# Performance work log

Measured on AMD Instinct MI355X. Metric: run time of the kernel, lower is better.

Reference implementation:

```python
import jax, jax.numpy as jnp
import numpy as np

B, S = 64, 1024
D_INPUT, D_POLAR, N_LAYERS, KAN, N_CLASSES = 256, 256, 8, 32, 1000
PI = float(np.pi)
EPS = 1e-8


def _gelu(v):
    return jax.nn.gelu(v, approximate=False)  # torch nn.GELU default = exact erf


def setup_inputs() -> dict:
    key = jax.random.key(0)
    ks = jax.random.split(key, 16)

    def rn(k, shape, fan_in):
        return jax.random.normal(k, shape, jnp.float32) / np.sqrt(fan_in)

    return {
        "x": jax.random.normal(ks[0], (B, S, D_INPUT), jnp.float32),
        "embed_w": rn(ks[1], (D_INPUT, 2 * D_POLAR), D_INPUT),
        "embed_b": jnp.zeros((2 * D_POLAR,), jnp.float32),
        "mag_w1": rn(ks[2], (N_LAYERS, 1, KAN), 1),
        "mag_b1": jnp.zeros((N_LAYERS, KAN), jnp.float32),
        "mag_w2": rn(ks[3], (N_LAYERS, KAN, 1), KAN),
        "mag_b2": jnp.zeros((N_LAYERS, 1), jnp.float32),
        "ph_w1": rn(ks[4], (N_LAYERS, 2, KAN), 2),
        "ph_b1": jnp.zeros((N_LAYERS, KAN), jnp.float32),
        "ph_w2": rn(ks[5], (N_LAYERS, KAN, 2), KAN),
        "ph_b2": jnp.zeros((N_LAYERS, 2), jnp.float32),
        "cls_w1": rn(ks[6], (D_POLAR, KAN), D_POLAR),
        "cls_b1": jnp.zeros((KAN,), jnp.float32),
        "cls_w2": rn(ks[7], (KAN, N_CLASSES), KAN),
        "cls_b2": jnp.zeros((N_CLASSES,), jnp.float32),
    }


def _forward(x, embed_w, embed_b, mag_w1, mag_b1, mag_w2, mag_b2,
             ph_w1, ph_b1, ph_w2, ph_b2, cls_w1, cls_b1, cls_w2, cls_b2):
    h = x @ embed_w + embed_b                      # [B,S,2D]
    r = jnp.abs(h[..., :D_POLAR]) + 0.1            # [B,S,D]
    theta = h[..., D_POLAR:] * PI                  # [B,S,D]
    for i in range(N_LAYERS):
        xc = r * jnp.cos(theta)
        yc = r * jnp.sin(theta)
        xm = xc.mean(axis=1, keepdims=True)        # [B,1,D]
        ym = yc.mean(axis=1, keepdims=True)
        r_agg = jnp.sqrt(xm * xm + ym * ym + EPS)
        th_agg = jnp.arctan2(ym, xm)
        # magnitude MLP (1 -> 32 -> 1) in log space, per channel
        log_r = jnp.log(r_agg + EPS)[..., None]    # [B,1,D,1]
        lr = _gelu(log_r @ mag_w1[i] + mag_b1[i]) @ mag_w2[i] + mag_b2[i]
        r_trans = jnp.exp(lr[..., 0])              # [B,1,D]
        # phase MLP (2 -> 32 -> 2) on (sin, cos)
        pin = jnp.stack([jnp.sin(th_agg), jnp.cos(th_agg)], axis=-1)  # [B,1,D,2]
        pout = _gelu(pin @ ph_w1[i] + ph_b1[i]) @ ph_w2[i] + ph_b2[i]
        norm = jnp.sqrt(pout[..., 0] ** 2 + pout[..., 1] ** 2 + EPS)
        th_trans = jnp.arctan2(pout[..., 0] / norm, pout[..., 1] / norm)
        x_out = xc + r_trans * jnp.cos(th_trans)
        y_out = yc + r_trans * jnp.sin(th_trans)
        r = jnp.sqrt(x_out * x_out + y_out * y_out + EPS)
        theta = jnp.arctan2(y_out, x_out)
    pooled = r.mean(axis=1)                        # [B,D]
    return _gelu(pooled @ cls_w1 + cls_b1) @ cls_w2 + cls_b2  # [B,n_classes]


def reference(x, embed_w, embed_b, mag_w1, mag_b1, mag_w2, mag_b2,
              ph_w1, ph_b1, ph_w2, ph_b2, cls_w1, cls_b1, cls_w2, cls_b2):
    return _forward(x, embed_w, embed_b, mag_w1, mag_b1, mag_w2, mag_b2,
                    ph_w1, ph_b1, ph_w2, ph_b2, cls_w1, cls_b1, cls_w2, cls_b2)
```

## Files before the change

kernel.cpp:

```cpp
#include <hip/hip_runtime.h>
#include <hip/hip_bf16.h>
#include <hip/hip_fp16.h>

#define EPS 1e-8f
#define PI_F 3.14159265358979323846f

typedef _Float16 half8 __attribute__((ext_vector_type(8)));
typedef _Float16 half4 __attribute__((ext_vector_type(4)));
typedef float f32x4 __attribute__((ext_vector_type(4)));
typedef float f32x2 __attribute__((ext_vector_type(2)));

__device__ __forceinline__ float gelu_exact(float v) {
    return 0.5f * v * (1.0f + erff(v * 0.70710678118654752f));
}

__global__ void convertW(const float* __restrict__ W,
                         _Float16* __restrict__ Wth, _Float16* __restrict__ Wtl,
                         float* __restrict__ zero_base) {
    int idx = blockIdx.x * 256 + threadIdx.x;
    if (idx < 49152) zero_base[idx] = 0.f;
    int col = idx & 511, k = idx >> 9;
    int d  = col & 255;
    int g  = d >> 6;
    int dl = d & 63;
    int r  = (dl >> 5) * 64 + ((col >> 8) << 5) + (dl & 31);
    int kt = k >> 5, ko = k & 31;
    float f = W[k * 512 + col];
    _Float16 h = (_Float16)f;
    int o = ((g * 8 + kt) * 128 + r) * 32 + ko;
    Wth[o] = h;
    Wtl[o] = (_Float16)(f - (float)h);
}

__global__ __launch_bounds__(256, 4) void gemm_embed(
    const float* __restrict__ x,
    const _Float16* __restrict__ Wth, const _Float16* __restrict__ Wtl,
    const float* __restrict__ bias,
    unsigned short* __restrict__ XY8,
    float* __restrict__ XMsum, float* __restrict__ YMsum)
{
    __shared__ __attribute__((aligned(16))) _Float16 Ah[4096], Al[4096];
    const int tid  = threadIdx.x;
    const int wave = tid >> 6;
    const int lane = tid & 63;
    const int wm   = wave >> 1;
    const int wn   = wave & 1;
    const int id   = blockIdx.x;
    const int xcd  = id & 7;
    const int s    = id >> 3;
    const int g    = s & 3;
    const int mt   = (s >> 2) * 8 + xcd;
    const int m0   = mt * 128;
    const int q    = lane >> 4, ln = lane & 15;

    f32x4 acc[4][4];
#pragma unroll
    for (int mi = 0; mi < 4; ++mi)
#pragma unroll
        for (int nt = 0; nt < 4; ++nt)
            acc[mi][nt] = (f32x4){0.f, 0.f, 0.f, 0.f};

    for (int kt = 0; kt < 8; ++kt) {
        half8 bh[4], bl[4];
        {
            const int tbase = (g * 8 + kt) * 4096;
#pragma unroll
            for (int nt = 0; nt < 4; ++nt) {
                int off = tbase + (wn * 64 + nt * 16 + ln) * 32 + q * 8;
                bh[nt] = *(const half8*)(Wth + off);
                bl[nt] = *(const half8*)(Wtl + off);
            }
        }
        __syncthreads();
#pragma unroll
        for (int L = 0; L < 2; ++L) {
            int idx2 = L * 256 + tid;
            int r = idx2 >> 2, cq = idx2 & 3;
            const float* src = x + (size_t)(m0 + r) * 256 + kt * 32 + cq * 8;
            const float4 f0 = *(const float4*)(src);
            const float4 f1 = *(const float4*)(src + 4);
            half8 hh, ll;
            hh[0] = (_Float16)f0.x; ll[0] = (_Float16)(f0.x - (float)hh[0]);
            hh[1] = (_Float16)f0.y; ll[1] = (_Float16)(f0.y - (float)hh[1]);
            hh[2] = (_Float16)f0.z; ll[2] = (_Float16)(f0.z - (float)hh[2]);
            hh[3] = (_Float16)f0.w; ll[3] = (_Float16)(f0.w - (float)hh[3]);
            hh[4] = (_Float16)f1.x; ll[4] = (_Float16)(f1.x - (float)hh[4]);
            hh[5] = (_Float16)f1.y; ll[5] = (_Float16)(f1.y - (float)hh[5]);
            hh[6] = (_Float16)f1.z; ll[6] = (_Float16)(f1.z - (float)hh[6]);
            hh[7] = (_Float16)f1.w; ll[7] = (_Float16)(f1.w - (float)hh[7]);
            int pos = cq ^ ((r >> 1) & 3);
            *(half8*)&Ah[r * 32 + pos * 8] = hh;
            *(half8*)&Al[r * 32 + pos * 8] = ll;
        }
        __syncthreads();

        half8 am[4];
#pragma unroll
        for (int mi = 0; mi < 4; ++mi) {
            int row = wm * 64 + mi * 16 + ln;
            am[mi] = *(const half8*)&Ah[row * 32 + (q ^ ((row >> 1) & 3)) * 8];
        }
#pragma unroll
        for (int mi = 0; mi < 4; ++mi)
#pragma unroll
            for (int nt = 0; nt < 4; ++nt)
                acc[mi][nt] = __builtin_amdgcn_mfma_f32_16x16x32_f16(am[mi], bh[nt], acc[mi][nt], 0, 0, 0);
#pragma unroll
        for (int mi = 0; mi < 4; ++mi)
#pragma unroll
            for (int nt = 0; nt < 4; ++nt)
                acc[mi][nt] = __builtin_amdgcn_mfma_f32_16x16x32_f16(am[mi], bl[nt], acc[mi][nt], 0, 0, 0);
#pragma unroll
        for (int mi = 0; mi < 4; ++mi) {
            int row = wm * 64 + mi * 16 + ln;
            half8 alv = *(const half8*)&Al[row * 32 + (q ^ ((row >> 1) & 3)) * 8];
#pragma unroll
            for (int nt = 0; nt < 4; ++nt)
                acc[mi][nt] = __builtin_amdgcn_mfma_f32_16x16x32_f16(alv, bh[nt], acc[mi][nt], 0, 0, 0);
        }
    }

    const int d0 = g * 64 + wn * 32 + ln;
    const int d1 = d0 + 16;
    const int b  = m0 >> 10;
    const float b1_0 = bias[d0],       b1_1 = bias[d1];
    const float b2_0 = bias[256 + d0], b2_1 = bias[256 + d1];
    float sx0 = 0.f, sy0 = 0.f, sx1 = 0.f, sy1 = 0.f;
#pragma unroll
    for (int mi = 0; mi < 4; ++mi) {
#pragma unroll
        for (int i = 0; i < 4; ++i) {
            const int row = m0 + wm * 64 + mi * 16 + q * 4 + i;
            {
                const float h1 = acc[mi][0][i] + b1_0;
                const float h2 = acc[mi][2][i] + b2_0;
                const float rr = fabsf(h1) + 0.1f;
                float sv, cv;
                __sincosf(PI_F * h2, &sv, &cv);
                const float xc = rr * cv, yc = rr * sv;
                int pk = __builtin_amdgcn_cvt_pk_fp8_f32(xc, yc, 0, false);
                XY8[(size_t)row * 256 + d0] = (unsigned short)pk;
                sx0 += xc; sy0 += yc;
            }
            {
                const float h1 = acc[mi][1][i] + b1_1;
                const float h2 = acc[mi][3][i] + b2_1;
                const float rr = fabsf(h1) + 0.1f;
                float sv, cv;
                __sincosf(PI_F * h2, &sv, &cv);
                const float xc = rr * cv, yc = rr * sv;
                int pk = __builtin_amdgcn_cvt_pk_fp8_f32(xc, yc, 0, false);
                XY8[(size_t)row * 256 + d1] = (unsigned short)pk;
                sx1 += xc; sy1 += yc;
            }
        }
    }
    sx0 += __shfl_down(sx0, 32); sx0 += __shfl_down(sx0, 16);
    sy0 += __shfl_down(sy0, 32); sy0 += __shfl_down(sy0, 16);
    sx1 += __shfl_down(sx1, 32); sx1 += __shfl_down(sx1, 16);
    sy1 += __shfl_down(sy1, 32); sy1 += __shfl_down(sy1, 16);
    if (lane < 16) {
        atomicAdd(&XMsum[b * 256 + d0], sx0);
        atomicAdd(&YMsum[b * 256 + d0], sy0);
        atomicAdd(&XMsum[b * 256 + d1], sx1);
        atomicAdd(&YMsum[b * 256 + d1], sy1);
    }
}

__global__ __launch_bounds__(256) void layers_kernel(
    const float* __restrict__ XMsum, const float* __restrict__ YMsum,
    const float* __restrict__ mw1, const float* __restrict__ mb1,
    const float* __restrict__ mw2, const float* __restrict__ mb2,
    const float* __restrict__ pw1, const float* __restrict__ pb1,
    const float* __restrict__ pw2, const float* __restrict__ pb2,
    float* __restrict__ DX, float* __restrict__ DY)
{
    __shared__ float s_mw1[256], s_mb1[256], s_mw2[256], s_mb2[8];
    __shared__ float s_pw1[512], s_pb1[256], s_pw2[512], s_pb2[16];
    const int tid = threadIdx.x;
    s_mw1[tid] = mw1[tid]; s_mb1[tid] = mb1[tid];
    s_mw2[tid] = mw2[tid]; s_pb1[tid] = pb1[tid];
    s_pw1[tid] = pw1[tid]; s_pw1[256 + tid] = pw1[256 + tid];
    s_pw2[tid] = pw2[tid]; s_pw2[256 + tid] = pw2[256 + tid];
    if (tid < 8)  s_mb2[tid] = mb2[tid];
    if (tid < 16) s_pb2[tid] = pb2[tid];
    __syncthreads();

    const int gid = blockIdx.x * 256 + tid;
    const int idx = gid >> 3;
    const int sub = gid & 7;
    float xm = XMsum[idx] * (1.0f / 1024.0f);
    float ym = YMsum[idx] * (1.0f / 1024.0f);
    float dxa = 0.f, dya = 0.f;
#pragma unroll 1
    for (int i = 0; i < 8; ++i) {
        float r2    = xm * xm + ym * ym;
        float r_agg = sqrtf(r2 + EPS);
        float hyp   = sqrtf(r2);
        float inv   = hyp > 0.f ? 1.0f / hyp : 0.f;
        float st    = ym * inv;
        float ct    = hyp > 0.f ? xm * inv : 1.0f;
        float log_r = logf(r_agg + EPS);
        float lr = 0.f, p0 = 0.f, p1 = 0.f;
#pragma unroll
        for (int k4 = 0; k4 < 4; ++k4) {
            int k = sub * 4 + k4;
            float hm = gelu_exact(log_r * s_mw1[i * 32 + k] + s_mb1[i * 32 + k]);
            lr += hm * s_mw2[i * 32 + k];
            float hp = gelu_exact(st * s_pw1[i * 64 + k] + ct * s_pw1[i * 64 + 32 + k] + s_pb1[i * 32 + k]);
            p0 += hp * s_pw2[i * 64 + 2 * k + 0];
            p1 += hp * s_pw2[i * 64 + 2 * k + 1];
        }
        lr += __shfl_xor(lr, 1); lr += __shfl_xor(lr, 2); lr += __shfl_xor(lr, 4);
        p0 += __shfl_xor(p0, 1); p0 += __shfl_xor(p0, 2); p0 += __shfl_xor(p0, 4);
        p1 += __shfl_xor(p1, 1); p1 += __shfl_xor(p1, 2); p1 += __shfl_xor(p1, 4);
        lr += s_mb2[i];
        p0 += s_pb2[i * 2 + 0];
        p1 += s_pb2[i * 2 + 1];
        float r_trans = expf(lr);
        float hp2  = sqrtf(p0 * p0 + p1 * p1);
        float invp = hp2 > 0.f ? 1.0f / hp2 : 0.f;
        float ctt  = hp2 > 0.f ? p1 * invp : 1.0f;
        float stt  = p0 * invp;
        float dx = r_trans * ctt;
        float dy = r_trans * stt;
        dxa += dx; dya += dy; xm += dx; ym += dy;
    }
    if (sub == 0) { DX[idx] = dxa; DY[idx] = dya; }
}

__global__ __launch_bounds__(256) void pool_kernel(
    const unsigned short* __restrict__ XY8,
    const float* __restrict__ DX, const float* __restrict__ DY,
    float* __restrict__ pooled)
{
    __shared__ float red[256][9];
    const int b = blockIdx.x, sc = blockIdx.y, tid = threadIdx.x;
    const int dg = tid & 31;
    const int sh = tid >> 5;
    const int d0 = dg * 8;
    float dxv[8], dyv[8], s[8];
#pragma unroll
    for (int j = 0; j < 8; ++j) {
        dxv[j] = DX[b * 256 + d0 + j];
        dyv[j] = DY[b * 256 + d0 + j];
        s[j] = 0.f;
    }
    const int r0 = sc * 128 + sh * 16;
    const size_t base = ((size_t)b * 1024 + r0) * 256 + d0;
#pragma unroll 4
    for (int i = 0; i < 16; ++i) {
        const int4 v = *(const int4*)(XY8 + base + (size_t)i * 256);
        const int wv[4] = {v.x, v.y, v.z, v.w};
#pragma unroll
        for (int w = 0; w < 4; ++w) {
            f32x2 pa = __builtin_amdgcn_cvt_pk_f32_fp8(wv[w], false);
            f32x2 pb = __builtin_amdgcn_cvt_pk_f32_fp8(wv[w], true);
            float xa = pa[0] + dxv[2 * w],     ya = pa[1] + dyv[2 * w];
            float xb = pb[0] + dxv[2 * w + 1], yb = pb[1] + dyv[2 * w + 1];
            s[2 * w]     += sqrtf(xa * xa + ya * ya + EPS);
            s[2 * w + 1] += sqrtf(xb * xb + yb * yb + EPS);
        }
    }
#pragma unroll
    for (int j = 0; j < 8; ++j) red[tid][j] = s[j];
    __syncthreads();
    if (tid < 32) {
#pragma unroll
        for (int j = 0; j < 8; ++j) {
            float t = 0.f;
#pragma unroll
            for (int c = 0; c < 8; ++c) t += red[c * 32 + tid][j];
            atomicAdd(&pooled[b * 256 + tid * 8 + j], t);
        }
    }
}

__global__ __launch_bounds__(256) void cls_kernel(
    const float* __restrict__ pooled,
    const float* __restrict__ w1, const float* __restrict__ b1,
    const float* __restrict__ w2, const float* __restrict__ b2,
    float* __restrict__ out)
{
    __shared__ float pl[256];
    __shared__ float part[8][32];
    __shared__ float hd[32];
    const int b = blockIdx.x, yc = blockIdx.y, tid = threadIdx.x;
    pl[tid] = pooled[b * 256 + tid] * (1.0f / 1024.0f);
    __syncthreads();
    const int hu = tid & 31, kc = tid >> 5;
    float a = 0.f;
    for (int k = kc * 32; k < kc * 32 + 32; ++k) a += pl[k] * w1[k * 32 + hu];
    part[kc][hu] = a;
    __syncthreads();
    if (tid < 32) {
        float s = b1[tid];
#pragma unroll
        for (int c = 0; c < 8; ++c) s += part[c][tid];
        hd[tid] = gelu_exact(s);
    }
    __syncthreads();
    const int n0 = yc * 250;
    const int nend = (n0 + 250 < 1000) ? n0 + 250 : 1000;
    for (int n = n0 + tid; n < nend; n += 256) {
        float s = b2[n];
#pragma unroll
        for (int k = 0; k < 32; ++k) s += hd[k] * w2[k * 1000 + n];
        out[b * 1000 + n] = s;
    }
}

extern "C" void kernel_launch(void* const* d_in, const int* in_sizes, int n_in,
                              void* d_out, int out_size, void* d_ws, size_t ws_size,
                              hipStream_t stream)
{
    const float* x       = (const float*)d_in[0];
    const float* embed_w = (const float*)d_in[1];
    const float* embed_b = (const float*)d_in[2];
    const float* mag_w1  = (const float*)d_in[3];
    const float* mag_b1  = (const float*)d_in[4];
    const float* mag_w2  = (const float*)d_in[5];
    const float* mag_b2  = (const float*)d_in[6];
    const float* ph_w1   = (const float*)d_in[7];
    const float* ph_b1   = (const float*)d_in[8];
    const float* ph_w2   = (const float*)d_in[9];
    const float* ph_b2   = (const float*)d_in[10];
    const float* cls_w1  = (const float*)d_in[11];
    const float* cls_b1  = (const float*)d_in[12];
    const float* cls_w2  = (const float*)d_in[13];
    const float* cls_b2  = (const float*)d_in[14];
    float* out = (float*)d_out;

    char* ws = (char*)d_ws;
    unsigned short* XY8 = (unsigned short*)(ws + 0);
    _Float16* Wth = (_Float16*)(ws + 33554432);
    _Float16* Wtl = (_Float16*)(ws + 33816576);
    float* XMsum  = (float*)(ws + 34078720);
    float* YMsum  = (float*)(ws + 34144256);
    float* pooled = (float*)(ws + 34209792);
    float* DX     = (float*)(ws + 34275328);
    float* DY     = (float*)(ws + 34340864);

    convertW<<<512, 256, 0, stream>>>(embed_w, Wth, Wtl, XMsum);
    gemm_embed<<<2048, 256, 0, stream>>>(x, Wth, Wtl, embed_b, XY8, XMsum, YMsum);
    layers_kernel<<<512, 256, 0, stream>>>(XMsum, YMsum, mag_w1, mag_b1, mag_w2, mag_b2,
                                           ph_w1, ph_b1, ph_w2, ph_b2, DX, DY);
    pool_kernel<<<dim3(64, 8), 256, 0, stream>>>(XY8, DX, DY, pooled);
    cls_kernel<<<dim3(64, 4), 256, 0, stream>>>(pooled, cls_w1, cls_b1, cls_w2, cls_b2, out);
}
```

Baseline: 204.2 us.

## Double-buffer embed GEMM LDS with register prefetch and pack paired fp8 stores

The embed GEMM now ping-pongs between two LDS buffers and prefetches the next k-tile of x into registers while the current tile is converted and consumed. This drops one barrier per k-step and hides global load latency. The weight column layout is permuted so each lane owns two adjacent channels, which lets the epilogue pack both channels' fp8 pairs into a single 32-bit store instead of two 16-bit stores. LDS use doubles and the launch bound drops from 4 to 3 blocks per CU, so occupancy may fall.

```diff
diff --git a/kernel.cpp b/kernel.cpp
--- a/kernel.cpp
+++ b/kernel.cpp
@@ -20,11 +20,12 @@
     int idx = blockIdx.x * 256 + threadIdx.x;
     if (idx < 49152) zero_base[idx] = 0.f;
     int col = idx & 511, k = idx >> 9;
-    int d  = col & 255;
-    int g  = d >> 6;
-    int dl = d & 63;
-    int r  = (dl >> 5) * 64 + ((col >> 8) << 5) + (dl & 31);
-    int kt = k >> 5, ko = k & 31;
+    int d   = col & 255;
+    int g   = d >> 6;
+    int dl  = d & 63;
+    int h12 = col >> 8;
+    int r   = (dl >> 5) * 64 + ((dl & 1) + 2 * h12) * 16 + ((dl & 31) >> 1);
+    int kt  = k >> 5, ko = k & 31;
     float f = W[k * 512 + col];
     _Float16 h = (_Float16)f;
     int o = ((g * 8 + kt) * 128 + r) * 32 + ko;
@@ -32,14 +33,14 @@
     Wtl[o] = (_Float16)(f - (float)h);
 }
 
-__global__ __launch_bounds__(256, 4) void gemm_embed(
+__global__ __launch_bounds__(256, 3) void gemm_embed(
     const float* __restrict__ x,
     const _Float16* __restrict__ Wth, const _Float16* __restrict__ Wtl,
     const float* __restrict__ bias,
     unsigned short* __restrict__ XY8,
     float* __restrict__ XMsum, float* __restrict__ YMsum)
 {
-    __shared__ __attribute__((aligned(16))) _Float16 Ah[4096], Al[4096];
+    __shared__ __attribute__((aligned(16))) _Float16 Ah[2][4096], Al[2][4096];
     const int tid  = threadIdx.x;
     const int wave = tid >> 6;
     const int lane = tid & 63;
@@ -60,99 +61,120 @@
         for (int nt = 0; nt < 4; ++nt)
             acc[mi][nt] = (f32x4){0.f, 0.f, 0.f, 0.f};
 
-    for (int kt = 0; kt < 8; ++kt) {
-        half8 bh[4], bl[4];
-        {
-            const int tbase = (g * 8 + kt) * 4096;
-#pragma unroll
-            for (int nt = 0; nt < 4; ++nt) {
-                int off = tbase + (wn * 64 + nt * 16 + ln) * 32 + q * 8;
-                bh[nt] = *(const half8*)(Wth + off);
-                bl[nt] = *(const half8*)(Wtl + off);
-            }
-        }
-        __syncthreads();
-#pragma unroll
-        for (int L = 0; L < 2; ++L) {
-            int idx2 = L * 256 + tid;
-            int r = idx2 >> 2, cq = idx2 & 3;
-            const float* src = x + (size_t)(m0 + r) * 256 + kt * 32 + cq * 8;
-            const float4 f0 = *(const float4*)(src);
-            const float4 f1 = *(const float4*)(src + 4);
-            half8 hh, ll;
-            hh[0] = (_Float16)f0.x; ll[0] = (_Float16)(f0.x - (float)hh[0]);
-            hh[1] = (_Float16)f0.y; ll[1] = (_Float16)(f0.y - (float)hh[1]);
-            hh[2] = (_Float16)f0.z; ll[2] = (_Float16)(f0.z - (float)hh[2]);
-            hh[3] = (_Float16)f0.w; ll[3] = (_Float16)(f0.w - (float)hh[3]);
-            hh[4] = (_Float16)f1.x; ll[4] = (_Float16)(f1.x - (float)hh[4]);
-            hh[5] = (_Float16)f1.y; ll[5] = (_Float16)(f1.y - (float)hh[5]);
-            hh[6] = (_Float16)f1.z; ll[6] = (_Float16)(f1.z - (float)hh[6]);
-            hh[7] = (_Float16)f1.w; ll[7] = (_Float16)(f1.w - (float)hh[7]);
-            int pos = cq ^ ((r >> 1) & 3);
-            *(half8*)&Ah[r * 32 + pos * 8] = hh;
-            *(half8*)&Al[r * 32 + pos * 8] = ll;
-        }
-        __syncthreads();
-
-        half8 am[4];
-#pragma unroll
-        for (int mi = 0; mi < 4; ++mi) {
-            int row = wm * 64 + mi * 16 + ln;
-            am[mi] = *(const half8*)&Ah[row * 32 + (q ^ ((row >> 1) & 3)) * 8];
-        }
-#pragma unroll
-        for (int mi = 0; mi < 4; ++mi)
-#pragma unroll
-            for (int nt = 0; nt < 4; ++nt)
-                acc[mi][nt] = __builtin_amdgcn_mfma_f32_16x16x32_f16(am[mi], bh[nt], acc[mi][nt], 0, 0, 0);
-#pragma unroll
-        for (int mi = 0; mi < 4; ++mi)
-#pragma unroll
-            for (int nt = 0; nt < 4; ++nt)
-                acc[mi][nt] = __builtin_amdgcn_mfma_f32_16x16x32_f16(am[mi], bl[nt], acc[mi][nt], 0, 0, 0);
-#pragma unroll
-        for (int mi = 0; mi < 4; ++mi) {
-            int row = wm * 64 + mi * 16 + ln;
-            half8 alv = *(const half8*)&Al[row * 32 + (q ^ ((row >> 1) & 3)) * 8];
-#pragma unroll
-            for (int nt = 0; nt < 4; ++nt)
-                acc[mi][nt] = __builtin_amdgcn_mfma_f32_16x16x32_f16(alv, bh[nt], acc[mi][nt], 0, 0, 0);
-        }
-    }
-
-    const int d0 = g * 64 + wn * 32 + ln;
-    const int d1 = d0 + 16;
+#define LOADX(KT, REG)                                                        \
+    {                                                                         \
+        _Pragma("unroll")                                                     \
+        for (int L = 0; L < 2; ++L) {                                         \
+            const int idx2 = L * 256 + tid;                                   \
+            const int rr_ = idx2 >> 2, cq_ = idx2 & 3;                        \
+            const float* src_ = x + (size_t)(m0 + rr_) * 256 + (KT) * 32 + cq_ * 8; \
+            REG[2 * L]     = *(const float4*)(src_);                          \
+            REG[2 * L + 1] = *(const float4*)(src_ + 4);                      \
+        }                                                                     \
+    }
+
+#define CVTWRITE(REG, BUF)                                                    \
+    {                                                                         \
+        _Pragma("unroll")                                                     \
+        for (int L = 0; L < 2; ++L) {                                         \
+            const int idx2 = L * 256 + tid;                                   \
+            const int rr_ = idx2 >> 2, cq_ = idx2 & 3;                        \
+            const float4 f0 = REG[2 * L], f1 = REG[2 * L + 1];                \
+            half8 hh, ll;                                                     \
+            hh[0] = (_Float16)f0.x; ll[0] = (_Float16)(f0.x - (float)hh[0]);  \
+            hh[1] = (_Float16)f0.y; ll[1] = (_Float16)(f0.y - (float)hh[1]);  \
+            hh[2] = (_Float16)f0.z; ll[2] = (_Float16)(f0.z - (float)hh[2]);  \
+            hh[3] = (_Float16)f0.w; ll[3] = (_Float16)(f0.w - (float)hh[3]);  \
+            hh[4] = (_Float16)f1.x; ll[4] = (_Float16)(f1.x - (float)hh[4]);  \
+            hh[5] = (_Float16)f1.y; ll[5] = (_Float16)(f1.y - (float)hh[5]);  \
+            hh[6] = (_Float16)f1.z; ll[6] = (_Float16)(f1.z - (float)hh[6]);  \
+            hh[7] = (_Float16)f1.w; ll[7] = (_Float16)(f1.w - (float)hh[7]);  \
+            const int pos_ = cq_ ^ ((rr_ >> 1) & 3);                          \
+            *(half8*)&Ah[BUF][rr_ * 32 + pos_ * 8] = hh;                      \
+            *(half8*)&Al[BUF][rr_ * 32 + pos_ * 8] = ll;                      \
+        }                                                                     \
+    }
+
+#define STEP(KT, CUR, NXT, BUF)                                               \
+    {                                                                         \
+        const int tbase_ = (g * 8 + (KT)) * 4096;                             \
+        half8 bh[4], bl[4];                                                   \
+        _Pragma("unroll")                                                     \
+        for (int nt = 0; nt < 4; ++nt) {                                      \
+            const int off_ = tbase_ + (wn * 64 + nt * 16 + ln) * 32 + q * 8;  \
+            bh[nt] = *(const half8*)(Wth + off_);                             \
+            bl[nt] = *(const half8*)(Wtl + off_);                             \
+        }                                                                     \
+        if ((KT) < 7) LOADX((KT) + 1, NXT);                                   \
+        CVTWRITE(CUR, BUF);                                                   \
+        asm volatile("s_waitcnt lgkmcnt(0)" ::: "memory");                    \
+        __builtin_amdgcn_s_barrier();                                         \
+        __builtin_amdgcn_sched_barrier(0);                                    \
+        half8 am[4];                                                          \
+        _Pragma("unroll")                                                     \
+        for (int mi = 0; mi < 4; ++mi) {                                      \
+            const int row_ = wm * 64 + mi * 16 + ln;                          \
+            am[mi] = *(const half8*)&Ah[BUF][row_ * 32 + (q ^ ((row_ >> 1) & 3)) * 8]; \
+        }                                                                     \
+        _Pragma("unroll")                                                     \
+        for (int mi = 0; mi < 4; ++mi)                                        \
+            _Pragma("unroll")                                                 \
+            for (int nt = 0; nt < 4; ++nt)                                    \
+                acc[mi][nt] = __builtin_amdgcn_mfma_f32_16x16x32_f16(am[mi], bh[nt], acc[mi][nt], 0, 0, 0); \
+        _Pragma("unroll")                                                     \
+        for (int mi = 0; mi < 4; ++mi)                                        \
+            _Pragma("unroll")                                                 \
+            for (int nt = 0; nt < 4; ++nt)                                    \
+                acc[mi][nt] = __builtin_amdgcn_mfma_f32_16x16x32_f16(am[mi], bl[nt], acc[mi][nt], 0, 0, 0); \
+        _Pragma("unroll")                                                     \
+        for (int mi = 0; mi < 4; ++mi) {                                      \
+            const int row_ = wm * 64 + mi * 16 + ln;                          \
+            const half8 alv = *(const half8*)&Al[BUF][row_ * 32 + (q ^ ((row_ >> 1) & 3)) * 8]; \
+            _Pragma("unroll")                                                 \
+            for (int nt = 0; nt < 4; ++nt)                                    \
+                acc[mi][nt] = __builtin_amdgcn_mfma_f32_16x16x32_f16(alv, bh[nt], acc[mi][nt], 0, 0, 0); \
+        }                                                                     \
+    }
+
+    float4 xA[4], xB[4];
+    LOADX(0, xA);
+#pragma unroll 1
+    for (int kp = 0; kp < 4; ++kp) {
+        const int kt0 = 2 * kp;
+        STEP(kt0,     xA, xB, 0);
+        STEP(kt0 + 1, xB, xA, 1);
+    }
+#undef LOADX
+#undef CVTWRITE
+#undef STEP
+
+    const int d0 = g * 64 + wn * 32 + 2 * ln;
     const int b  = m0 >> 10;
-    const float b1_0 = bias[d0],       b1_1 = bias[d1];
-    const float b2_0 = bias[256 + d0], b2_1 = bias[256 + d1];
+    const float b1_0 = bias[d0],       b1_1 = bias[d0 + 1];
+    const float b2_0 = bias[256 + d0], b2_1 = bias[256 + d0 + 1];
     float sx0 = 0.f, sy0 = 0.f, sx1 = 0.f, sy1 = 0.f;
 #pragma unroll
     for (int mi = 0; mi < 4; ++mi) {
 #pragma unroll
         for (int i = 0; i < 4; ++i) {
             const int row = m0 + wm * 64 + mi * 16 + q * 4 + i;
-            {
-                const float h1 = acc[mi][0][i] + b1_0;
-                const float h2 = acc[mi][2][i] + b2_0;
-                const float rr = fabsf(h1) + 0.1f;
-                float sv, cv;
-                __sincosf(PI_F * h2, &sv, &cv);
-                const float xc = rr * cv, yc = rr * sv;
-                int pk = __builtin_amdgcn_cvt_pk_fp8_f32(xc, yc, 0, false);
-                XY8[(size_t)row * 256 + d0] = (unsigned short)pk;
-                sx0 += xc; sy0 += yc;
-            }
-            {
-                const float h1 = acc[mi][1][i] + b1_1;
-                const float h2 = acc[mi][3][i] + b2_1;
-                const float rr = fabsf(h1) + 0.1f;
-                float sv, cv;
-                __sincosf(PI_F * h2, &sv, &cv);
-                const float xc = rr * cv, yc = rr * sv;
-                int pk = __builtin_amdgcn_cvt_pk_fp8_f32(xc, yc, 0, false);
-                XY8[(size_t)row * 256 + d1] = (unsigned short)pk;
-                sx1 += xc; sy1 += yc;
-            }
+            const float h1a = acc[mi][0][i] + b1_0;
+            const float h2a = acc[mi][2][i] + b2_0;
+            const float rra = fabsf(h1a) + 0.1f;
+            float sva, cva;
+            __sincosf(PI_F * h2a, &sva, &cva);
+            const float xca = rra * cva, yca = rra * sva;
+            const float h1b = acc[mi][1][i] + b1_1;
+            const float h2b = acc[mi][3][i] + b2_1;
+            const float rrb = fabsf(h1b) + 0.1f;
+            float svb, cvb;
+            __sincosf(PI_F * h2b, &svb, &cvb);
+            const float xcb = rrb * cvb, ycb = rrb * svb;
+            int pk = __builtin_amdgcn_cvt_pk_fp8_f32(xca, yca, 0, false);
+            pk = __builtin_amdgcn_cvt_pk_fp8_f32(xcb, ycb, pk, true);
+            *(unsigned int*)(XY8 + (size_t)row * 256 + d0) = (unsigned int)pk;
+            sx0 += xca; sy0 += yca;
+            sx1 += xcb; sy1 += ycb;
         }
     }
     sx0 += __shfl_down(sx0, 32); sx0 += __shfl_down(sx0, 16);
@@ -162,8 +184,8 @@
     if (lane < 16) {
         atomicAdd(&XMsum[b * 256 + d0], sx0);
         atomicAdd(&YMsum[b * 256 + d0], sy0);
-        atomicAdd(&XMsum[b * 256 + d1], sx1);
-        atomicAdd(&YMsum[b * 256 + d1], sy1);
+        atomicAdd(&XMsum[b * 256 + d0 + 1], sx1);
+        atomicAdd(&YMsum[b * 256 + d0 + 1], sy1);
     }
 }
 
```

After: 211.2 us. 1.03x slower.

## Load A operands directly from global into registers and pack paired channel stores

Applied to the files above, without the earlier changes.

The embed GEMM no longer stages the x tile through shared memory. Each wave loads its own A fragments straight from global memory, splits them into fp16 hi/lo in registers, and so drops both __syncthreads and the LDS traffic. The weight layout is remapped so each lane owns two adjacent channels, which lets the epilogue write both fp8 pairs as one 32-bit store. The occupancy hint in launch_bounds is removed. The cost is that adjacent waves (the two wn waves) each reload and reconvert the same x rows, and the stores and loads are less coalesced than the cooperative tile load.

```diff
diff --git a/kernel.cpp b/kernel.cpp
--- a/kernel.cpp
+++ b/kernel.cpp
@@ -20,11 +20,12 @@
     int idx = blockIdx.x * 256 + threadIdx.x;
     if (idx < 49152) zero_base[idx] = 0.f;
     int col = idx & 511, k = idx >> 9;
-    int d  = col & 255;
-    int g  = d >> 6;
-    int dl = d & 63;
-    int r  = (dl >> 5) * 64 + ((col >> 8) << 5) + (dl & 31);
-    int kt = k >> 5, ko = k & 31;
+    int d   = col & 255;
+    int g   = d >> 6;
+    int dl  = d & 63;
+    int h12 = col >> 8;
+    int r   = (dl >> 5) * 64 + ((dl & 1) + 2 * h12) * 16 + ((dl & 31) >> 1);
+    int kt  = k >> 5, ko = k & 31;
     float f = W[k * 512 + col];
     _Float16 h = (_Float16)f;
     int o = ((g * 8 + kt) * 128 + r) * 32 + ko;
@@ -32,14 +33,13 @@
     Wtl[o] = (_Float16)(f - (float)h);
 }
 
-__global__ __launch_bounds__(256, 4) void gemm_embed(
+__global__ __launch_bounds__(256) void gemm_embed(
     const float* __restrict__ x,
     const _Float16* __restrict__ Wth, const _Float16* __restrict__ Wtl,
     const float* __restrict__ bias,
     unsigned short* __restrict__ XY8,
     float* __restrict__ XMsum, float* __restrict__ YMsum)
 {
-    __shared__ __attribute__((aligned(16))) _Float16 Ah[4096], Al[4096];
     const int tid  = threadIdx.x;
     const int wave = tid >> 6;
     const int lane = tid & 63;
@@ -60,23 +60,25 @@
         for (int nt = 0; nt < 4; ++nt)
             acc[mi][nt] = (f32x4){0.f, 0.f, 0.f, 0.f};
 
+    const float* xbase[4];
+#pragma unroll
+    for (int mi = 0; mi < 4; ++mi)
+        xbase[mi] = x + (size_t)(m0 + wm * 64 + mi * 16 + ln) * 256 + q * 8;
+
+    const _Float16* wb = Wth + (size_t)g * 32768 + (wn * 64 + ln) * 32 + q * 8;
+    const _Float16* wl = Wtl + (size_t)g * 32768 + (wn * 64 + ln) * 32 + q * 8;
+
+#pragma unroll 1
     for (int kt = 0; kt < 8; ++kt) {
         half8 bh[4], bl[4];
-        {
-            const int tbase = (g * 8 + kt) * 4096;
-#pragma unroll
-            for (int nt = 0; nt < 4; ++nt) {
-                int off = tbase + (wn * 64 + nt * 16 + ln) * 32 + q * 8;
-                bh[nt] = *(const half8*)(Wth + off);
-                bl[nt] = *(const half8*)(Wtl + off);
-            }
-        }
-        __syncthreads();
-#pragma unroll
-        for (int L = 0; L < 2; ++L) {
-            int idx2 = L * 256 + tid;
-            int r = idx2 >> 2, cq = idx2 & 3;
-            const float* src = x + (size_t)(m0 + r) * 256 + kt * 32 + cq * 8;
+#pragma unroll
+        for (int nt = 0; nt < 4; ++nt) {
+            bh[nt] = *(const half8*)(wb + kt * 4096 + nt * 512);
+            bl[nt] = *(const half8*)(wl + kt * 4096 + nt * 512);
+        }
+#pragma unroll
+        for (int mi = 0; mi < 4; ++mi) {
+            const float* src = xbase[mi] + kt * 32;
             const float4 f0 = *(const float4*)(src);
             const float4 f1 = *(const float4*)(src + 4);
             half8 hh, ll;
@@ -88,71 +90,45 @@
             hh[5] = (_Float16)f1.y; ll[5] = (_Float16)(f1.y - (float)hh[5]);
             hh[6] = (_Float16)f1.z; ll[6] = (_Float16)(f1.z - (float)hh[6]);
             hh[7] = (_Float16)f1.w; ll[7] = (_Float16)(f1.w - (float)hh[7]);
-            int pos = cq ^ ((r >> 1) & 3);
-            *(half8*)&Ah[r * 32 + pos * 8] = hh;
-            *(half8*)&Al[r * 32 + pos * 8] = ll;
-        }
-        __syncthreads();
-
-        half8 am[4];
-#pragma unroll
-        for (int mi = 0; mi < 4; ++mi) {
-            int row = wm * 64 + mi * 16 + ln;
-            am[mi] = *(const half8*)&Ah[row * 32 + (q ^ ((row >> 1) & 3)) * 8];
-        }
-#pragma unroll
-        for (int mi = 0; mi < 4; ++mi)
 #pragma unroll
             for (int nt = 0; nt < 4; ++nt)
-                acc[mi][nt] = __builtin_amdgcn_mfma_f32_16x16x32_f16(am[mi], bh[nt], acc[mi][nt], 0, 0, 0);
-#pragma unroll
-        for (int mi = 0; mi < 4; ++mi)
+                acc[mi][nt] = __builtin_amdgcn_mfma_f32_16x16x32_f16(hh, bh[nt], acc[mi][nt], 0, 0, 0);
 #pragma unroll
             for (int nt = 0; nt < 4; ++nt)
-                acc[mi][nt] = __builtin_amdgcn_mfma_f32_16x16x32_f16(am[mi], bl[nt], acc[mi][nt], 0, 0, 0);
-#pragma unroll
-        for (int mi = 0; mi < 4; ++mi) {
-            int row = wm * 64 + mi * 16 + ln;
-            half8 alv = *(const half8*)&Al[row * 32 + (q ^ ((row >> 1) & 3)) * 8];
+                acc[mi][nt] = __builtin_amdgcn_mfma_f32_16x16x32_f16(hh, bl[nt], acc[mi][nt], 0, 0, 0);
 #pragma unroll
             for (int nt = 0; nt < 4; ++nt)
-                acc[mi][nt] = __builtin_amdgcn_mfma_f32_16x16x32_f16(alv, bh[nt], acc[mi][nt], 0, 0, 0);
-        }
-    }
-
-    const int d0 = g * 64 + wn * 32 + ln;
-    const int d1 = d0 + 16;
+                acc[mi][nt] = __builtin_amdgcn_mfma_f32_16x16x32_f16(ll, bh[nt], acc[mi][nt], 0, 0, 0);
+        }
+    }
+
+    const int d0 = g * 64 + wn * 32 + 2 * ln;
     const int b  = m0 >> 10;
-    const float b1_0 = bias[d0],       b1_1 = bias[d1];
-    const float b2_0 = bias[256 + d0], b2_1 = bias[256 + d1];
+    const float b1_0 = bias[d0],       b1_1 = bias[d0 + 1];
+    const float b2_0 = bias[256 + d0], b2_1 = bias[256 + d0 + 1];
     float sx0 = 0.f, sy0 = 0.f, sx1 = 0.f, sy1 = 0.f;
 #pragma unroll
     for (int mi = 0; mi < 4; ++mi) {
 #pragma unroll
         for (int i = 0; i < 4; ++i) {
             const int row = m0 + wm * 64 + mi * 16 + q * 4 + i;
-            {
-                const float h1 = acc[mi][0][i] + b1_0;
-                const float h2 = acc[mi][2][i] + b2_0;
-                const float rr = fabsf(h1) + 0.1f;
-                float sv, cv;
-                __sincosf(PI_F * h2, &sv, &cv);
-                const float xc = rr * cv, yc = rr * sv;
-                int pk = __builtin_amdgcn_cvt_pk_fp8_f32(xc, yc, 0, false);
-                XY8[(size_t)row * 256 + d0] = (unsigned short)pk;
-                sx0 += xc; sy0 += yc;
-            }
-            {
-                const float h1 = acc[mi][1][i] + b1_1;
-                const float h2 = acc[mi][3][i] + b2_1;
-                const float rr = fabsf(h1) + 0.1f;
-                float sv, cv;
-                __sincosf(PI_F * h2, &sv, &cv);
-                const float xc = rr * cv, yc = rr * sv;
-                int pk = __builtin_amdgcn_cvt_pk_fp8_f32(xc, yc, 0, false);
-                XY8[(size_t)row * 256 + d1] = (unsigned short)pk;
-                sx1 += xc; sy1 += yc;
-            }
+            const float h1a = acc[mi][0][i] + b1_0;
+            const float h2a = acc[mi][2][i] + b2_0;
+            const float rra = fabsf(h1a) + 0.1f;
+            float sva, cva;
+            __sincosf(PI_F * h2a, &sva, &cva);
+            const float xca = rra * cva, yca = rra * sva;
+            const float h1b = acc[mi][1][i] + b1_1;
+            const float h2b = acc[mi][3][i] + b2_1;
+            const float rrb = fabsf(h1b) + 0.1f;
+            float svb, cvb;
+            __sincosf(PI_F * h2b, &svb, &cvb);
+            const float xcb = rrb * cvb, ycb = rrb * svb;
+            int pk = __builtin_amdgcn_cvt_pk_fp8_f32(xca, yca, 0, false);
+            pk = __builtin_amdgcn_cvt_pk_fp8_f32(xcb, ycb, pk, true);
+            *(unsigned int*)(XY8 + (size_t)row * 256 + d0) = (unsigned int)pk;
+            sx0 += xca; sy0 += yca;
+            sx1 += xcb; sy1 += ycb;
         }
     }
     sx0 += __shfl_down(sx0, 32); sx0 += __shfl_down(sx0, 16);
@@ -162,8 +138,8 @@
     if (lane < 16) {
         atomicAdd(&XMsum[b * 256 + d0], sx0);
         atomicAdd(&YMsum[b * 256 + d0], sy0);
-        atomicAdd(&XMsum[b * 256 + d1], sx1);
-        atomicAdd(&YMsum[b * 256 + d1], sy1);
+        atomicAdd(&XMsum[b * 256 + d0 + 1], sx1);
+        atomicAdd(&YMsum[b * 256 + d0 + 1], sy1);
     }
 }
 
```

After: 239.5 us. +17.3%, slower.

## Fuse layer-MLP kernel with pooling kernel into one tail kernel

Applied to the files above, without the earlier changes.

Merges the per-channel 8-layer MLP computation and the pooling pass into a single kernel, one block per (batch, 64-channel quarter). Each block computes the displacement DX/DY for its 64 channels in shared memory, then scans all 1024 rows for those channels and writes pooled sums directly without atomics. This removes a kernel launch, the DX/DY global round-trip, and the atomic adds. The cost is fewer blocks for the pooling phase (256 instead of 512) and each thread now runs the MLP loop twice, which may reduce parallelism.

```diff
diff --git a/kernel.cpp b/kernel.cpp
--- a/kernel.cpp
+++ b/kernel.cpp
@@ -6,7 +6,6 @@
 #define PI_F 3.14159265358979323846f
 
 typedef _Float16 half8 __attribute__((ext_vector_type(8)));
-typedef _Float16 half4 __attribute__((ext_vector_type(4)));
 typedef float f32x4 __attribute__((ext_vector_type(4)));
 typedef float f32x2 __attribute__((ext_vector_type(2)));
 
@@ -167,17 +166,21 @@
     }
 }
 
-__global__ __launch_bounds__(256) void layers_kernel(
+__global__ __launch_bounds__(256) void tail_kernel(
     const float* __restrict__ XMsum, const float* __restrict__ YMsum,
     const float* __restrict__ mw1, const float* __restrict__ mb1,
     const float* __restrict__ mw2, const float* __restrict__ mb2,
     const float* __restrict__ pw1, const float* __restrict__ pb1,
     const float* __restrict__ pw2, const float* __restrict__ pb2,
-    float* __restrict__ DX, float* __restrict__ DY)
+    const unsigned short* __restrict__ XY8,
+    float* __restrict__ pooled)
 {
     __shared__ float s_mw1[256], s_mb1[256], s_mw2[256], s_mb2[8];
     __shared__ float s_pw1[512], s_pb1[256], s_pw2[512], s_pb2[16];
-    const int tid = threadIdx.x;
+    __shared__ float dxl[64], dyl[64];
+    __shared__ float red[256][9];
+    const int b = blockIdx.x, qd = blockIdx.y, tid = threadIdx.x;
+
     s_mw1[tid] = mw1[tid]; s_mb1[tid] = mb1[tid];
     s_mw2[tid] = mw2[tid]; s_pb1[tid] = pb1[tid];
     s_pw1[tid] = pw1[tid]; s_pw1[256 + tid] = pw1[256 + tid];
@@ -186,93 +189,89 @@
     if (tid < 16) s_pb2[tid] = pb2[tid];
     __syncthreads();
 
-    const int gid = blockIdx.x * 256 + tid;
-    const int idx = gid >> 3;
-    const int sub = gid & 7;
-    float xm = XMsum[idx] * (1.0f / 1024.0f);
-    float ym = YMsum[idx] * (1.0f / 1024.0f);
-    float dxa = 0.f, dya = 0.f;
 #pragma unroll 1
-    for (int i = 0; i < 8; ++i) {
-        float r2    = xm * xm + ym * ym;
-        float r_agg = sqrtf(r2 + EPS);
-        float hyp   = sqrtf(r2);
-        float inv   = hyp > 0.f ? 1.0f / hyp : 0.f;
-        float st    = ym * inv;
-        float ct    = hyp > 0.f ? xm * inv : 1.0f;
-        float log_r = logf(r_agg + EPS);
-        float lr = 0.f, p0 = 0.f, p1 = 0.f;
-#pragma unroll
-        for (int k4 = 0; k4 < 4; ++k4) {
-            int k = sub * 4 + k4;
-            float hm = gelu_exact(log_r * s_mw1[i * 32 + k] + s_mb1[i * 32 + k]);
-            lr += hm * s_mw2[i * 32 + k];
-            float hp = gelu_exact(st * s_pw1[i * 64 + k] + ct * s_pw1[i * 64 + 32 + k] + s_pb1[i * 32 + k]);
-            p0 += hp * s_pw2[i * 64 + 2 * k + 0];
-            p1 += hp * s_pw2[i * 64 + 2 * k + 1];
-        }
-        lr += __shfl_xor(lr, 1); lr += __shfl_xor(lr, 2); lr += __shfl_xor(lr, 4);
-        p0 += __shfl_xor(p0, 1); p0 += __shfl_xor(p0, 2); p0 += __shfl_xor(p0, 4);
-        p1 += __shfl_xor(p1, 1); p1 += __shfl_xor(p1, 2); p1 += __shfl_xor(p1, 4);
-        lr += s_mb2[i];
-        p0 += s_pb2[i * 2 + 0];
-        p1 += s_pb2[i * 2 + 1];
-        float r_trans = expf(lr);
-        float hp2  = sqrtf(p0 * p0 + p1 * p1);
-        float invp = hp2 > 0.f ? 1.0f / hp2 : 0.f;
-        float ctt  = hp2 > 0.f ? p1 * invp : 1.0f;
-        float stt  = p0 * invp;
-        float dx = r_trans * ctt;
-        float dy = r_trans * stt;
-        dxa += dx; dya += dy; xm += dx; ym += dy;
-    }
-    if (sub == 0) { DX[idx] = dxa; DY[idx] = dya; }
-}
-
-__global__ __launch_bounds__(256) void pool_kernel(
-    const unsigned short* __restrict__ XY8,
-    const float* __restrict__ DX, const float* __restrict__ DY,
-    float* __restrict__ pooled)
-{
-    __shared__ float red[256][9];
-    const int b = blockIdx.x, sc = blockIdx.y, tid = threadIdx.x;
-    const int dg = tid & 31;
-    const int sh = tid >> 5;
-    const int d0 = dg * 8;
-    float dxv[8], dyv[8], s[8];
-#pragma unroll
-    for (int j = 0; j < 8; ++j) {
-        dxv[j] = DX[b * 256 + d0 + j];
-        dyv[j] = DY[b * 256 + d0 + j];
-        s[j] = 0.f;
-    }
-    const int r0 = sc * 128 + sh * 16;
-    const size_t base = ((size_t)b * 1024 + r0) * 256 + d0;
+    for (int it = 0; it < 2; ++it) {
+        const int u    = it * 256 + tid;
+        const int sub  = u & 7;
+        const int dloc = u >> 3;
+        const int idx  = b * 256 + qd * 64 + dloc;
+        float xm = XMsum[idx] * (1.0f / 1024.0f);
+        float ym = YMsum[idx] * (1.0f / 1024.0f);
+        float dxa = 0.f, dya = 0.f;
+#pragma unroll 1
+        for (int i = 0; i < 8; ++i) {
+            float r2    = xm * xm + ym * ym;
+            float r_agg = sqrtf(r2 + EPS);
+            float hyp   = sqrtf(r2);
+            float inv   = hyp > 0.f ? 1.0f / hyp : 0.f;
+            float st    = ym * inv;
+            float ct    = hyp > 0.f ? xm * inv : 1.0f;
+            float log_r = logf(r_agg + EPS);
+            float lr = 0.f, p0 = 0.f, p1 = 0.f;
+#pragma unroll
+            for (int k4 = 0; k4 < 4; ++k4) {
+                int k = sub * 4 + k4;
+                float hm = gelu_exact(log_r * s_mw1[i * 32 + k] + s_mb1[i * 32 + k]);
+                lr += hm * s_mw2[i * 32 + k];
+                float hp = gelu_exact(st * s_pw1[i * 64 + k] + ct * s_pw1[i * 64 + 32 + k] + s_pb1[i * 32 + k]);
+                p0 += hp * s_pw2[i * 64 + 2 * k + 0];
+                p1 += hp * s_pw2[i * 64 + 2 * k + 1];
+            }
+            lr += __shfl_xor(lr, 1); lr += __shfl_xor(lr, 2); lr += __shfl_xor(lr, 4);
+            p0 += __shfl_xor(p0, 1); p0 += __shfl_xor(p0, 2); p0 += __shfl_xor(p0, 4);
+            p1 += __shfl_xor(p1, 1); p1 += __shfl_xor(p1, 2); p1 += __shfl_xor(p1, 4);
+            lr += s_mb2[i];
+            p0 += s_pb2[i * 2 + 0];
+            p1 += s_pb2[i * 2 + 1];
+            float r_trans = expf(lr);
+            float hp2  = sqrtf(p0 * p0 + p1 * p1);
+            float invp = hp2 > 0.f ? 1.0f / hp2 : 0.f;
+            float ctt  = hp2 > 0.f ? p1 * invp : 1.0f;
+            float stt  = p0 * invp;
+            float dx = r_trans * ctt;
+            float dy = r_trans * stt;
+            dxa += dx; dya += dy; xm += dx; ym += dy;
+        }
+        if (sub == 0) { dxl[dloc] = dxa; dyl[dloc] = dya; }
+    }
+    __syncthreads();
+
+    {
+        const int dg = tid & 7;
+        const int sh = tid >> 3;
+        const int d0 = qd * 64 + dg * 8;
+        float dxv[8], dyv[8], sacc[8];
+#pragma unroll
+        for (int j = 0; j < 8; ++j) {
+            dxv[j] = dxl[dg * 8 + j];
+            dyv[j] = dyl[dg * 8 + j];
+            sacc[j] = 0.f;
+        }
+        const size_t base = ((size_t)b * 1024 + sh * 32) * 256 + d0;
 #pragma unroll 4
-    for (int i = 0; i < 16; ++i) {
-        const int4 v = *(const int4*)(XY8 + base + (size_t)i * 256);
-        const int wv[4] = {v.x, v.y, v.z, v.w};
-#pragma unroll
-        for (int w = 0; w < 4; ++w) {
-            f32x2 pa = __builtin_amdgcn_cvt_pk_f32_fp8(wv[w], false);
-            f32x2 pb = __builtin_amdgcn_cvt_pk_f32_fp8(wv[w], true);
-            float xa = pa[0] + dxv[2 * w],     ya = pa[1] + dyv[2 * w];
-            float xb = pb[0] + dxv[2 * w + 1], yb = pb[1] + dyv[2 * w + 1];
-            s[2 * w]     += sqrtf(xa * xa + ya * ya + EPS);
-            s[2 * w + 1] += sqrtf(xb * xb + yb * yb + EPS);
-        }
-    }
-#pragma unroll
-    for (int j = 0; j < 8; ++j) red[tid][j] = s[j];
-    __syncthreads();
-    if (tid < 32) {
-#pragma unroll
-        for (int j = 0; j < 8; ++j) {
-            float t = 0.f;
-#pragma unroll
-            for (int c = 0; c < 8; ++c) t += red[c * 32 + tid][j];
-            atomicAdd(&pooled[b * 256 + tid * 8 + j], t);
-        }
+        for (int i = 0; i < 32; ++i) {
+            const int4 v = *(const int4*)(XY8 + base + (size_t)i * 256);
+            const int wv[4] = {v.x, v.y, v.z, v.w};
+#pragma unroll
+            for (int w = 0; w < 4; ++w) {
+                f32x2 pa = __builtin_amdgcn_cvt_pk_f32_fp8(wv[w], false);
+                f32x2 pb = __builtin_amdgcn_cvt_pk_f32_fp8(wv[w], true);
+                float xa = pa[0] + dxv[2 * w],     ya = pa[1] + dyv[2 * w];
+                float xb = pb[0] + dxv[2 * w + 1], yb = pb[1] + dyv[2 * w + 1];
+                sacc[2 * w]     += sqrtf(xa * xa + ya * ya + EPS);
+                sacc[2 * w + 1] += sqrtf(xb * xb + yb * yb + EPS);
+            }
+        }
+#pragma unroll
+        for (int j = 0; j < 8; ++j) red[tid][j] = sacc[j];
+    }
+    __syncthreads();
+    if (tid < 64) {
+        const int dgq = tid >> 3, j = tid & 7;
+        float t = 0.f;
+#pragma unroll
+        for (int c = 0; c < 32; ++c) t += red[c * 8 + dgq][j];
+        pooled[b * 256 + qd * 64 + dgq * 8 + j] = t;
     }
 }
 
@@ -338,13 +337,12 @@
     float* XMsum  = (float*)(ws + 34078720);
     float* YMsum  = (float*)(ws + 34144256);
     float* pooled = (float*)(ws + 34209792);
-    float* DX     = (float*)(ws + 34275328);
-    float* DY     = (float*)(ws + 34340864);
 
     convertW<<<512, 256, 0, stream>>>(embed_w, Wth, Wtl, XMsum);
     gemm_embed<<<2048, 256, 0, stream>>>(x, Wth, Wtl, embed_b, XY8, XMsum, YMsum);
-    layers_kernel<<<512, 256, 0, stream>>>(XMsum, YMsum, mag_w1, mag_b1, mag_w2, mag_b2,
-                                           ph_w1, ph_b1, ph_w2, ph_b2, DX, DY);
-    pool_kernel<<<dim3(64, 8), 256, 0, stream>>>(XY8, DX, DY, pooled);
+    tail_kernel<<<dim3(64, 4), 256, 0, stream>>>(XMsum, YMsum,
+                                                 mag_w1, mag_b1, mag_w2, mag_b2,
+                                                 ph_w1, ph_b1, ph_w2, ph_b2,
+                                                 XY8, pooled);
     cls_kernel<<<dim3(64, 4), 256, 0, stream>>>(pooled, cls_w1, cls_b1, cls_w2, cls_b2, out);
 }
```

Result: slower. 209.1 us (+2.4%).
